# Optimization experiments

Hardware: AMD Instinct MI355X
Metric: run time of the kernel (lower is better)

Reference implementation:

```python
import jax, jax.numpy as jnp
import numpy as np
jax.config.update("jax_enable_x64", True)

B, S, E, H, L, FF = 2, 1024, 768, 12, 4, 2048
MAX_THOUGHT_LEN = 3
LN_EPS = 1e-5

def _sinusoidal_pe(max_len, d):
    pos = np.arange(max_len)[:, None]
    div = np.exp(np.arange(0, d, 2) * (-np.log(10000.0) / d))
    pe = np.zeros((max_len, d), np.float32)
    pe[:, 0::2] = np.sin(pos * div)
    pe[:, 1::2] = np.cos(pos * div)
    return jnp.asarray(pe)

def _build_mask(Smax, thoughts_taken, n_tokens):
    # Vectorized equivalent of the torch loop building the block-causal mask.
    bs = thoughts_taken + 1
    i = np.arange(Smax)[:, None]
    j = np.arange(Smax)[None, :]
    same_block = (i // bs == j // bs) & (i // bs < n_tokens) & ((i % bs) >= (j % bs))
    start_vis = ((j % bs) == 0) & (j // bs < n_tokens) & (i > j) & (i < n_tokens * bs)
    allowed = same_block | start_vis
    # TransformerEncoder canonicalizes the bool mask: True (disallowed) -> -inf additive
    return jnp.asarray(np.where(allowed, 0.0, -np.inf).astype(np.float64))

def _layernorm(x, w, b):
    mu = jnp.mean(x, -1, keepdims=True)
    var = jnp.mean((x - mu) ** 2, -1, keepdims=True)
    return (x - mu) / jnp.sqrt(var + LN_EPS) * w + b

def setup_inputs() -> dict:
    key = jax.random.key(0)
    ks = jax.random.split(key, 8)
    f32 = jnp.float32
    return {
        "x": jax.random.normal(ks[0], (B, S, E), f32),
        "padding_mask": jnp.zeros((B, S), bool),
        "thought_pe": jax.random.normal(ks[1], (MAX_THOUGHT_LEN + 1, E), f32),
        "Wqkv": jax.random.normal(ks[2], (L, 3 * E, E), f32) * (E ** -0.5),
        "bqkv": jnp.zeros((L, 3 * E), f32),
        "W1": jax.random.normal(ks[3], (L, FF, E), f32) * (E ** -0.5),
        "b1": jnp.zeros((L, FF), f32),
        "W2": jax.random.normal(ks[4], (L, E, FF), f32) * (FF ** -0.5),
        "b2": jnp.zeros((L, E), f32),
        "ln1_w": jnp.ones((L, E), f32), "ln1_b": jnp.zeros((L, E), f32),
        "ln2_w": jnp.ones((L, E), f32), "ln2_b": jnp.zeros((L, E), f32),
        "lnf_w": jnp.ones((E,), f32), "lnf_b": jnp.zeros((E,), f32),
        "thoughts_taken": 1,
        "real_token_count": 512,
    }

def reference(x, padding_mask, thought_pe, Wqkv, bqkv, W1, b1, W2, b2,
              ln1_w, ln1_b, ln2_w, ln2_b, lnf_w, lnf_b,
              thoughts_taken, real_token_count):
    # NOTE: padding_mask is accepted but unused, matching the custom layer.
    nt = thoughts_taken + 1
    pe = _sinusoidal_pe(S, E)
    # DualPositionalEncoding (eval mode -> dropout is identity)
    h = x[:, : real_token_count * nt].reshape(B, real_token_count, nt, E)
    h = h + pe[:real_token_count][None, :, None, :] + thought_pe[:nt][None, None, :, :]
    h = h.reshape(B, real_token_count * nt, E)
    pad = S - real_token_count * nt
    if pad > 0:
        h = jnp.pad(h, ((0, 0), (0, pad), (0, 0)))
    mask = _build_mask(S, thoughts_taken, real_token_count)
    scale = 1.0 / jnp.sqrt(jnp.float64(E // H))
    for l in range(L):
        # manual fp64 attention, exactly as the torch layer
        s64 = h.astype(jnp.float64)
        qkv = s64 @ Wqkv[l].astype(jnp.float64).T + bqkv[l].astype(jnp.float64)
        q, k, v = jnp.split(qkv, 3, axis=-1)
        rh = lambda t: t.reshape(B, S, H, E // H).transpose(0, 2, 1, 3)
        q, k, v = rh(q), rh(k), rh(v)
        scores = jnp.einsum("bhqd,bhkd->bhqk", q, k) * scale + mask
        attn = jax.nn.softmax(scores, axis=-1)
        ao = jnp.einsum("bhqk,bhkd->bhqd", attn, v).transpose(0, 2, 1, 3).reshape(B, S, E)
        # NOTE: no out_proj -- the custom forward skips self_attn.out_proj
        h = _layernorm(h + ao.astype(h.dtype), ln1_w[l], ln1_b[l])
        ff = jax.nn.gelu(h @ W1[l].T + b1[l], approximate=False) @ W2[l].T + b2[l]
        h = _layernorm(h + ff, ln2_w[l], ln2_b[l])
        h = jnp.nan_to_num(h)
    return _layernorm(h, lnf_w, lnf_b)
```

## Files before the change

### kernel.cpp

```cpp
#include <hip/hip_runtime.h>
#include <math.h>

#define SEQ 1024
#define EMB 768
#define NHEAD 12
#define HDIM 64
#define NLAYER 4
#define FFDIM 2048
#define BATCH 2
#define ROWS (BATCH * SEQ)
#define BH (BATCH * NHEAD)
#define NCHUNK 4

using f16 = _Float16;
using f16x4 = __attribute__((ext_vector_type(4))) _Float16;
using f16x8 = __attribute__((ext_vector_type(8))) _Float16;
using f32x4 = __attribute__((ext_vector_type(4))) float;
using f32x16 = __attribute__((ext_vector_type(16))) float;
typedef unsigned long long u64;

__device__ inline void gload16(const void* g, void* l) {
    __builtin_amdgcn_global_load_lds((const __attribute__((address_space(1))) unsigned*)g,
                                     (__attribute__((address_space(3))) unsigned*)l, 16, 0, 0);
}

__global__ void embed_kernel(const float* __restrict__ x,
                             const float* __restrict__ tpe,
                             float* __restrict__ h32,
                             f16* __restrict__ h16,
                             const int* __restrict__ tt_p,
                             const int* __restrict__ rtc_p) {
    int idx = blockIdx.x * blockDim.x + threadIdx.x;
    if (idx >= BATCH * SEQ * EMB) return;
    int e = idx % EMB;
    int s = (idx / EMB) % SEQ;
    int nt = *tt_p + 1;
    int rtc = *rtc_p;
    float val;
    if (s < rtc * nt) {
        int p = s / nt;
        int t = s % nt;
        int i2 = e & ~1;
        float div = __expf((float)i2 * -0.0119926314f);
        float ang = (float)p * div;
        float pe = (e & 1) ? __cosf(ang) : __sinf(ang);
        val = x[idx] + pe + tpe[t * EMB + e];
    } else {
        val = 0.0f;
    }
    h32[idx] = val;
    h16[idx] = (f16)val;
}

__global__ void build_mask(u64* __restrict__ mtab,
                           const int* __restrict__ tt_p,
                           const int* __restrict__ rtc_p) {
    int idx = blockIdx.x * blockDim.x + threadIdx.x;
    if (idx >= SEQ * 16) return;
    int i = idx >> 4, jt = idx & 15;
    int nt = *tt_p + 1, rtc = *rtc_p;
    int id = i / nt, im = i % nt;
    int iok = (i < rtc * nt);
    u64 m = 0;
    for (int k = 0; k < 64; k++) {
        int j = jt * 64 + k;
        int jd = j / nt, jm = j % nt;
        bool same = (id == jd) && (id < rtc) && (im >= jm);
        bool sv   = (jm == 0) && (jd < rtc) && (i > j) && iok;
        if (same || sv) m |= (1ull << k);
    }
    mtab[idx] = m;
}

__global__ void cast3(const float* __restrict__ a, int na,
                      const float* __restrict__ b, int nb,
                      const float* __restrict__ c, int nc,
                      f16* __restrict__ oa, f16* __restrict__ ob, f16* __restrict__ oc) {
    int total = na + nb + nc;
    for (int i = blockIdx.x * blockDim.x + threadIdx.x; i < total;
         i += gridDim.x * blockDim.x) {
        const float* src;
        f16* dst;
        int off;
        if (i < na)            { src = a; dst = oa; off = i; }
        else if (i < na + nb)  { src = b; dst = ob; off = i - na; }
        else                   { src = c; dst = oc; off = i - na - nb; }
        float4 v = ((const float4*)src)[off];
        f16x4 o;
        o[0] = (f16)v.x; o[1] = (f16)v.y; o[2] = (f16)v.z; o[3] = (f16)v.w;
        ((f16x4*)dst)[off] = o;
    }
}

template<int ACT, int OUT>
__global__ __launch_bounds__(256) void gemm_f16(const f16* __restrict__ A,
                                                const f16* __restrict__ W,
                                                const float* __restrict__ bias,
                                                f16* __restrict__ Ch,
                                                f16* __restrict__ vtg,
                                                int M, int N, int K) {
    __shared__ f16 As[2][128 * 64];
    __shared__ f16 Ws[2][128 * 64];
    const int tid = threadIdx.x, lane = tid & 63, wave = tid >> 6;
    const int gx = gridDim.x;
    const int nwg = gx * gridDim.y;
    int orig = blockIdx.y * gx + blockIdx.x;
    int nid = (nwg & 7) ? orig : ((orig & 7) * (nwg >> 3) + (orig >> 3));
    const int bm = (nid / gx) * 128, bn = (nid % gx) * 128;
    const int l31 = lane & 31, l32 = lane >> 5;
    const int wm = (wave >> 1) * 64, wn = (wave & 1) * 64;
    const int srow = lane >> 3, sslot = lane & 7;
    const int klen = K / gridDim.z;
    const int kbeg = blockIdx.z * klen;
    const int nsteps = klen >> 6;

    f32x16 acc[2][2];
#pragma unroll
    for (int mi = 0; mi < 2; mi++)
#pragma unroll
        for (int ni = 0; ni < 2; ni++)
#pragma unroll
            for (int e = 0; e < 16; e++) acc[mi][ni][e] = 0.f;

#pragma unroll
    for (int i = 0; i < 4; i++) {
        int R0 = wave * 32 + i * 8;
        int row = R0 + srow;
        int gs = (sslot ^ (row & 7)) << 3;
        gload16(A + (size_t)(bm + row) * K + kbeg + gs, As[0] + R0 * 64);
        gload16(W + (size_t)(bn + row) * K + kbeg + gs, Ws[0] + R0 * 64);
    }
    __syncthreads();

    int cur = 0;
    for (int t = 0; t < nsteps; t++) {
        if (t + 1 < nsteps) {
            int k1 = kbeg + (t + 1) * 64;
            int nxt = cur ^ 1;
#pragma unroll
            for (int i = 0; i < 4; i++) {
                int R0 = wave * 32 + i * 8;
                int row = R0 + srow;
                int gs = (sslot ^ (row & 7)) << 3;
                gload16(A + (size_t)(bm + row) * K + k1 + gs, As[nxt] + R0 * 64);
                gload16(W + (size_t)(bn + row) * K + k1 + gs, Ws[nxt] + R0 * 64);
            }
        }
#pragma unroll
        for (int ks = 0; ks < 4; ks++) {
            int kslot = ks * 2 + l32;
            f16x8 a[2], b[2];
#pragma unroll
            for (int mi = 0; mi < 2; mi++) {
                int row = wm + mi * 32 + l31;
                a[mi] = *(const f16x8*)(As[cur] + row * 64 + ((kslot ^ (row & 7)) << 3));
            }
#pragma unroll
            for (int ni = 0; ni < 2; ni++) {
                int row = wn + ni * 32 + l31;
                b[ni] = *(const f16x8*)(Ws[cur] + row * 64 + ((kslot ^ (row & 7)) << 3));
            }
#pragma unroll
            for (int mi = 0; mi < 2; mi++)
#pragma unroll
                for (int ni = 0; ni < 2; ni++)
                    acc[mi][ni] = __builtin_amdgcn_mfma_f32_32x32x16_f16(a[mi], b[ni], acc[mi][ni], 0, 0, 0);
        }
        __syncthreads();
        cur ^= 1;
    }

#pragma unroll
    for (int ni = 0; ni < 2; ni++) {
        int nbase = bn + wn + ni * 32;
        int n = nbase + l31;
        if (OUT == 3) {
            f16* dst = Ch + (size_t)blockIdx.z * ROWS * N;
#pragma unroll
            for (int mi = 0; mi < 2; mi++)
#pragma unroll
                for (int reg = 0; reg < 16; reg++) {
                    int m = bm + wm + mi * 32 + (reg & 3) + 8 * (reg >> 2) + 4 * l32;
                    dst[(size_t)m * N + n] = (f16)acc[mi][ni][reg];
                }
        } else {
            float bv = bias[n];
            if (OUT != 2 || nbase < 2 * EMB) {
                int cstride = (OUT == 2) ? 2 * EMB : N;
#pragma unroll
                for (int mi = 0; mi < 2; mi++) {
#pragma unroll
                    for (int reg = 0; reg < 16; reg++) {
                        int m = bm + wm + mi * 32 + (reg & 3) + 8 * (reg >> 2) + 4 * l32;
                        float v = acc[mi][ni][reg] + bv;
                        if (ACT) v = 0.5f * v * (1.0f + erff(v * 0.70710678118654752f));
                        Ch[(size_t)m * cstride + n] = (f16)v;
                    }
                }
            } else {
                int d = n - 2 * EMB;
                int hh = d >> 6, dd = d & 63;
#pragma unroll
                for (int mi = 0; mi < 2; mi++) {
#pragma unroll
                    for (int q = 0; q < 4; q++) {
                        int m0 = bm + wm + mi * 32 + 8 * q + 4 * l32;
                        int bb = m0 >> 10, s0 = m0 & (SEQ - 1);
                        f16x4 pack;
#pragma unroll
                        for (int r = 0; r < 4; r++) pack[r] = (f16)(acc[mi][ni][4 * q + r] + bv);
                        *(f16x4*)(vtg + ((size_t)((bb * NHEAD + hh) * HDIM + dd)) * SEQ + s0) = pack;
                    }
                }
            }
        }
    }
}

__global__ __launch_bounds__(256) void attn_part(const f16* __restrict__ qk,
                                                 const f16* __restrict__ vtg,
                                                 const u64* __restrict__ mtab,
                                                 f16* __restrict__ po,
                                                 float* __restrict__ pm,
                                                 float* __restrict__ pl) {
    const int c = blockIdx.x;
    const int qt = blockIdx.y;
    if (c * 4 > qt) return;
    const int bh = blockIdx.z;
    const int b = bh / NHEAD, hh = bh % NHEAD;
    const int q0 = qt * 64;
    const int jt_beg = c * 4, jt_end = min(qt, c * 4 + 3);

    __shared__ f16 Qs[64 * 64];
    __shared__ f16 Ks[2][64 * 64];
    __shared__ f16 VT[2][64 * 64];
    __shared__ f16 Ps[4 * 16 * 64];

    const int tid = threadIdx.x, lane = tid & 63, wave = tid >> 6;
    const int l15 = lane & 15, l16 = lane >> 4;
    const int RS = 2 * EMB;
    const f16* vth = vtg + (size_t)(b * NHEAD + hh) * HDIM * SEQ;
    const float SCALE2 = 0.125f * 1.44269504088896f;

#pragma unroll
    for (int it = 0; it < 2; it++) {
        int R0 = wave * 16 + it * 8;
        int row = R0 + (lane >> 3), slot = lane & 7;
        int gs = (slot ^ (row & 7)) << 3;
        gload16(qk + (size_t)(b * SEQ + q0 + row) * RS + hh * HDIM + gs, Qs + R0 * 64);
        gload16(qk + (size_t)(b * SEQ + jt_beg * 64 + row) * RS + EMB + hh * HDIM + gs,
                Ks[0] + R0 * 64);
        gload16(vth + (size_t)row * SEQ + jt_beg * 64 + gs, VT[0] + R0 * 64);
    }
    __syncthreads();

    f16x8 qa[2];
#pragma unroll
    for (int ks = 0; ks < 2; ks++) {
        int row = wave * 16 + l15;
        int kslot = l16 + ks * 4;
        qa[ks] = *(const f16x8*)(Qs + row * 64 + ((kslot ^ (row & 7)) << 3));
    }

    float mrow[4], lsum[4];
    f32x4 o[4];
    int iglob[4];
#pragma unroll
    for (int r = 0; r < 4; r++) {
        mrow[r] = -1e30f; lsum[r] = 0.f;
        iglob[r] = q0 + wave * 16 + l16 * 4 + r;
    }
#pragma unroll
    for (int nf = 0; nf < 4; nf++) o[nf] = (f32x4){0.f, 0.f, 0.f, 0.f};

    for (int jt = jt_beg; jt <= jt_end; jt++) {
        const int cur = (jt - jt_beg) & 1;
        if (jt < jt_end) {
            const int nxt = cur ^ 1;
            const int jn0 = (jt + 1) * 64;
#pragma unroll
            for (int it = 0; it < 2; it++) {
                int R0 = wave * 16 + it * 8;
                int row = R0 + (lane >> 3), slot = lane & 7;
                int gs = (slot ^ (row & 7)) << 3;
                gload16(qk + (size_t)(b * SEQ + jn0 + row) * RS + EMB + hh * HDIM + gs,
                        Ks[nxt] + R0 * 64);
                gload16(vth + (size_t)row * SEQ + jn0 + gs, VT[nxt] + R0 * 64);
            }
        }

        unsigned mlo[4], mhi[4];
#pragma unroll
        for (int r = 0; r < 4; r++) {
            u64 mk = mtab[iglob[r] * 16 + jt];
            mlo[r] = (unsigned)mk;
            mhi[r] = (unsigned)(mk >> 32);
        }

        f32x4 s[4];
        __builtin_amdgcn_s_setprio(1);
#pragma unroll
        for (int nf = 0; nf < 4; nf++) {
            s[nf] = (f32x4){0.f, 0.f, 0.f, 0.f};
#pragma unroll
            for (int ks = 0; ks < 2; ks++) {
                int row = nf * 16 + l15;
                int kslot = l16 + ks * 4;
                f16x8 kb = *(const f16x8*)(Ks[cur] + row * 64 + ((kslot ^ (row & 7)) << 3));
                s[nf] = __builtin_amdgcn_mfma_f32_16x16x32_f16(qa[ks], kb, s[nf], 0, 0, 0);
            }
        }
        __builtin_amdgcn_s_setprio(0);

        float p[4][4];
        float tmax[4] = {-1e30f, -1e30f, -1e30f, -1e30f};
#pragma unroll
        for (int nf = 0; nf < 4; nf++) {
            int sh = (nf & 1) * 16 + l15;
#pragma unroll
            for (int r = 0; r < 4; r++) {
                unsigned w = (nf & 2) ? mhi[r] : mlo[r];
                bool allowed = (w >> sh) & 1;
                float val = allowed ? s[nf][r] * SCALE2 : -1e30f;
                p[nf][r] = val;
                tmax[r] = fmaxf(tmax[r], val);
            }
        }
#pragma unroll
        for (int r = 0; r < 4; r++) {
            tmax[r] = fmaxf(tmax[r], __shfl_xor(tmax[r], 1));
            tmax[r] = fmaxf(tmax[r], __shfl_xor(tmax[r], 2));
            tmax[r] = fmaxf(tmax[r], __shfl_xor(tmax[r], 4));
            tmax[r] = fmaxf(tmax[r], __shfl_xor(tmax[r], 8));
        }
        float alpha[4], rsum[4], meff[4];
#pragma unroll
        for (int r = 0; r < 4; r++) {
            float mn = fmaxf(mrow[r], tmax[r]);
            alpha[r] = exp2f(mrow[r] - mn);
            mrow[r] = mn;
            meff[r] = (mn <= -1e29f) ? 0.f : mn;
            rsum[r] = 0.f;
        }
#pragma unroll
        for (int nf = 0; nf < 4; nf++)
#pragma unroll
            for (int r = 0; r < 4; r++) {
                float e = exp2f(p[nf][r] - meff[r]);
                p[nf][r] = e;
                rsum[r] += e;
            }
#pragma unroll
        for (int r = 0; r < 4; r++) {
            rsum[r] += __shfl_xor(rsum[r], 1);
            rsum[r] += __shfl_xor(rsum[r], 2);
            rsum[r] += __shfl_xor(rsum[r], 4);
            rsum[r] += __shfl_xor(rsum[r], 8);
            lsum[r] = lsum[r] * alpha[r] + rsum[r];
        }
#pragma unroll
        for (int nf = 0; nf < 4; nf++)
#pragma unroll
            for (int r = 0; r < 4; r++) o[nf][r] *= alpha[r];

        f16* P = Ps + wave * 16 * 64;
#pragma unroll
        for (int nf = 0; nf < 4; nf++)
#pragma unroll
            for (int r = 0; r < 4; r++) {
                int prow = l16 * 4 + r;
                int pcol = nf * 16 + l15;
                P[prow * 64 + (((pcol >> 3) ^ (prow & 7)) << 3) + (pcol & 7)] = (f16)p[nf][r];
            }

        __builtin_amdgcn_s_setprio(1);
#pragma unroll
        for (int ks = 0; ks < 2; ks++) {
            int kslot = l16 + ks * 4;
            int prow = l15;
            f16x8 pa = *(const f16x8*)(P + prow * 64 + ((kslot ^ (prow & 7)) << 3));
#pragma unroll
            for (int nf = 0; nf < 4; nf++) {
                int vrow = nf * 16 + l15;
                f16x8 vb = *(const f16x8*)(VT[cur] + vrow * 64 + ((kslot ^ (vrow & 7)) << 3));
                o[nf] = __builtin_amdgcn_mfma_f32_16x16x32_f16(pa, vb, o[nf], 0, 0, 0);
            }
        }
        __builtin_amdgcn_s_setprio(0);
        __syncthreads();
    }

    const size_t base = (size_t)(c * BH + bh) * SEQ;
#pragma unroll
    for (int r = 0; r < 4; r++) {
        int i = q0 + wave * 16 + l16 * 4 + r;
#pragma unroll
        for (int nf = 0; nf < 4; nf++)
            po[(base + i) * 64 + nf * 16 + l15] = (f16)o[nf][r];
        if (l15 == 0) {
            pm[base + i] = mrow[r];
            pl[base + i] = lsum[r];
        }
    }
}

__global__ __launch_bounds__(256) void add_ln_attn(const float* __restrict__ X,
                                                   const f16* __restrict__ po,
                                                   const float* __restrict__ pm,
                                                   const float* __restrict__ pl,
                                                   const float* __restrict__ w,
                                                   const float* __restrict__ bsh,
                                                   float* __restrict__ out32,
                                                   f16* __restrict__ out16) {
    const int row = blockIdx.x * 4 + (threadIdx.x >> 6);
    const int lane = threadIdx.x & 63;
    const int b = row >> 10, i = row & (SEQ - 1);
    const int nch = (i >> 6) / 4 + 1;
    const float* xr = X + (size_t)row * EMB;
    float4 v[3];
    float s = 0.f;
#pragma unroll
    for (int t = 0; t < 3; t++) {
        int e = t * 256 + lane * 4;
        int hh = e >> 6, d = e & 63;
        size_t hbase = (size_t)(b * NHEAD + hh) * SEQ + i;
        float m = -1e30f;
        for (int c = 0; c < nch; c++) m = fmaxf(m, pm[hbase + (size_t)c * BH * SEQ]);
        float meff = (m <= -1e29f) ? 0.f : m;
        float lt = 0.f;
        float4 ov = {0.f, 0.f, 0.f, 0.f};
        for (int c = 0; c < nch; c++) {
            size_t idx = hbase + (size_t)c * BH * SEQ;
            float wgt = exp2f(pm[idx] - meff);
            lt += pl[idx] * wgt;
            f16x4 pv = *(const f16x4*)(po + idx * 64 + d);
            ov.x += (float)pv[0] * wgt; ov.y += (float)pv[1] * wgt;
            ov.z += (float)pv[2] * wgt; ov.w += (float)pv[3] * wgt;
        }
        float inv = (lt > 0.f) ? 1.0f / lt : 0.0f;
        float4 a = *(const float4*)(xr + e);
        a.x += ov.x * inv; a.y += ov.y * inv; a.z += ov.z * inv; a.w += ov.w * inv;
        v[t] = a;
        s += a.x + a.y + a.z + a.w;
    }
#pragma unroll
    for (int k = 1; k < 64; k <<= 1) s += __shfl_xor(s, k);
    float mu = s * (1.0f / EMB);
    float s2 = 0.f;
#pragma unroll
    for (int t = 0; t < 3; t++) {
        float dx = v[t].x - mu, dy = v[t].y - mu, dz = v[t].z - mu, dw = v[t].w - mu;
        s2 += dx * dx + dy * dy + dz * dz + dw * dw;
    }
#pragma unroll
    for (int k = 1; k < 64; k <<= 1) s2 += __shfl_xor(s2, k);
    float inv = rsqrtf(s2 * (1.0f / EMB) + 1e-5f);
#pragma unroll
    for (int t = 0; t < 3; t++) {
        int e = t * 256 + lane * 4;
        float4 wv = *(const float4*)(w + e);
        float4 bv = *(const float4*)(bsh + e);
        float4 o;
        o.x = (v[t].x - mu) * inv * wv.x + bv.x;
        o.y = (v[t].y - mu) * inv * wv.y + bv.y;
        o.z = (v[t].z - mu) * inv * wv.z + bv.z;
        o.w = (v[t].w - mu) * inv * wv.w + bv.w;
        *(float4*)(out32 + (size_t)row * EMB + e) = o;
        f16x4 hh;
        hh[0] = (f16)o.x; hh[1] = (f16)o.y; hh[2] = (f16)o.z; hh[3] = (f16)o.w;
        *(f16x4*)(out16 + (size_t)row * EMB + e) = hh;
    }
}

__global__ __launch_bounds__(256) void add_ln_split4(const float* __restrict__ X,
                                                     const f16* __restrict__ part,
                                                     const float* __restrict__ bias,
                                                     const float* __restrict__ w,
                                                     const float* __restrict__ bsh,
                                                     float* __restrict__ out32,
                                                     f16* __restrict__ out16) {
    const int row = blockIdx.x * 4 + (threadIdx.x >> 6);
    const int lane = threadIdx.x & 63;
    const float* xr = X + (size_t)row * EMB;
    float4 v[3];
    float s = 0.f;
#pragma unroll
    for (int t = 0; t < 3; t++) {
        int e = t * 256 + lane * 4;
        float4 a = *(const float4*)(xr + e);
        float4 bb = *(const float4*)(bias + e);
        a.x += bb.x; a.y += bb.y; a.z += bb.z; a.w += bb.w;
#pragma unroll
        for (int z = 0; z < 4; z++) {
            f16x4 pz = *(const f16x4*)(part + (size_t)z * ROWS * EMB + (size_t)row * EMB + e);
            a.x += (float)pz[0]; a.y += (float)pz[1];
            a.z += (float)pz[2]; a.w += (float)pz[3];
        }
        v[t] = a;
        s += a.x + a.y + a.z + a.w;
    }
#pragma unroll
    for (int k = 1; k < 64; k <<= 1) s += __shfl_xor(s, k);
    float mu = s * (1.0f / EMB);
    float s2 = 0.f;
#pragma unroll
    for (int t = 0; t < 3; t++) {
        float dx = v[t].x - mu, dy = v[t].y - mu, dz = v[t].z - mu, dw = v[t].w - mu;
        s2 += dx * dx + dy * dy + dz * dz + dw * dw;
    }
#pragma unroll
    for (int k = 1; k < 64; k <<= 1) s2 += __shfl_xor(s2, k);
    float inv = rsqrtf(s2 * (1.0f / EMB) + 1e-5f);
#pragma unroll
    for (int t = 0; t < 3; t++) {
        int e = t * 256 + lane * 4;
        float4 wv = *(const float4*)(w + e);
        float4 bv = *(const float4*)(bsh + e);
        float4 o;
        o.x = (v[t].x - mu) * inv * wv.x + bv.x;
        o.y = (v[t].y - mu) * inv * wv.y + bv.y;
        o.z = (v[t].z - mu) * inv * wv.z + bv.z;
        o.w = (v[t].w - mu) * inv * wv.w + bv.w;
        *(float4*)(out32 + (size_t)row * EMB + e) = o;
        f16x4 hh;
        hh[0] = (f16)o.x; hh[1] = (f16)o.y; hh[2] = (f16)o.z; hh[3] = (f16)o.w;
        *(f16x4*)(out16 + (size_t)row * EMB + e) = hh;
    }
}

__global__ __launch_bounds__(256) void ln_final(const float* __restrict__ X,
                                                const float* __restrict__ w,
                                                const float* __restrict__ bsh,
                                                float* __restrict__ out32) {
    const int row = blockIdx.x * 4 + (threadIdx.x >> 6);
    const int lane = threadIdx.x & 63;
    const float* xr = X + (size_t)row * EMB;
    float4 v[3];
    float s = 0.f;
#pragma unroll
    for (int t = 0; t < 3; t++) {
        int e = t * 256 + lane * 4;
        v[t] = *(const float4*)(xr + e);
        s += v[t].x + v[t].y + v[t].z + v[t].w;
    }
#pragma unroll
    for (int k = 1; k < 64; k <<= 1) s += __shfl_xor(s, k);
    float mu = s * (1.0f / EMB);
    float s2 = 0.f;
#pragma unroll
    for (int t = 0; t < 3; t++) {
        float dx = v[t].x - mu, dy = v[t].y - mu, dz = v[t].z - mu, dw = v[t].w - mu;
        s2 += dx * dx + dy * dy + dz * dz + dw * dw;
    }
#pragma unroll
    for (int k = 1; k < 64; k <<= 1) s2 += __shfl_xor(s2, k);
    float inv = rsqrtf(s2 * (1.0f / EMB) + 1e-5f);
#pragma unroll
    for (int t = 0; t < 3; t++) {
        int e = t * 256 + lane * 4;
        float4 wv = *(const float4*)(w + e);
        float4 bv = *(const float4*)(bsh + e);
        float4 o;
        o.x = (v[t].x - mu) * inv * wv.x + bv.x;
        o.y = (v[t].y - mu) * inv * wv.y + bv.y;
        o.z = (v[t].z - mu) * inv * wv.z + bv.z;
        o.w = (v[t].w - mu) * inv * wv.w + bv.w;
        *(float4*)(out32 + (size_t)row * EMB + e) = o;
    }
}

extern "C" void kernel_launch(void* const* d_in, const int* in_sizes, int n_in,
                              void* d_out, int out_size, void* d_ws, size_t ws_size,
                              hipStream_t stream) {
    const float* x      = (const float*)d_in[0];
    const float* tpe    = (const float*)d_in[2];
    const float* Wqkv   = (const float*)d_in[3];
    const float* bqkv   = (const float*)d_in[4];
    const float* W1     = (const float*)d_in[5];
    const float* b1     = (const float*)d_in[6];
    const float* W2     = (const float*)d_in[7];
    const float* b2     = (const float*)d_in[8];
    const float* ln1_w  = (const float*)d_in[9];
    const float* ln1_b  = (const float*)d_in[10];
    const float* ln2_w  = (const float*)d_in[11];
    const float* ln2_b  = (const float*)d_in[12];
    const float* lnf_w  = (const float*)d_in[13];
    const float* lnf_b  = (const float*)d_in[14];
    const int*   tt     = (const int*)d_in[15];
    const int*   rtc    = (const int*)d_in[16];
    float* out = (float*)d_out;

    char* wsp = (char*)d_ws;
    float* h32  = (float*)wsp;
    f16*   h16  = (f16*)(wsp + 6291456);
    f16*   act  = (f16*)(wsp + 9437184);
    f16*   vtg  = (f16*)(wsp + 17825792);
    f16*   part = (f16*)(wsp + 20971520);
    f16*   wbuf = (f16*)(wsp + 33554432);
    f16*   po   = (f16*)(wsp + 72876032);
    float* pm   = (float*)(wsp + 85458944);
    float* pl   = (float*)(wsp + 85852160);
    u64*   mtab = (u64*)(wsp + 86245376);

    const int EQ = 3 * EMB * EMB;
    const int E1 = FFDIM * EMB;
    const int E2 = EMB * FFDIM;
    f16* wqAll = wbuf;
    f16* w1All = wbuf + (size_t)NLAYER * EQ;
    f16* w2All = w1All + (size_t)NLAYER * E1;

    cast3<<<4096, 256, 0, stream>>>(Wqkv, NLAYER * EQ / 4, W1, NLAYER * E1 / 4,
                                    W2, NLAYER * E2 / 4, wqAll, w1All, w2All);
    embed_kernel<<<(BATCH * SEQ * EMB + 255) / 256, 256, 0, stream>>>(x, tpe, h32, h16, tt, rtc);
    build_mask<<<SEQ * 16 / 256, 256, 0, stream>>>(mtab, tt, rtc);

    for (int l = 0; l < NLAYER; l++) {
        const f16* wq16 = wqAll + (size_t)l * EQ;
        const f16* w116 = w1All + (size_t)l * E1;
        const f16* w216 = w2All + (size_t)l * E2;
        const float* bq  = bqkv + (size_t)l * 3 * EMB;
        const float* bb1 = b1 + (size_t)l * FFDIM;
        const float* bb2 = b2 + (size_t)l * EMB;

        gemm_f16<0, 2><<<dim3(3 * EMB / 128, ROWS / 128), 256, 0, stream>>>(
            h16, wq16, bq, act, vtg, ROWS, 3 * EMB, EMB);

        attn_part<<<dim3(NCHUNK, SEQ / 64, BH), 256, 0, stream>>>(act, vtg, mtab, po, pm, pl);

        add_ln_attn<<<ROWS / 4, 256, 0, stream>>>(h32, po, pm, pl,
                                                  ln1_w + l * EMB, ln1_b + l * EMB, h32, h16);

        gemm_f16<1, 1><<<dim3(FFDIM / 128, ROWS / 128), 256, 0, stream>>>(
            h16, w116, bb1, act, nullptr, ROWS, FFDIM, EMB);

        gemm_f16<0, 3><<<dim3(EMB / 128, ROWS / 128, 4), 256, 0, stream>>>(
            act, w216, nullptr, part, nullptr, ROWS, EMB, FFDIM);

        add_ln_split4<<<ROWS / 4, 256, 0, stream>>>(h32, part, bb2,
                                                    ln2_w + l * EMB, ln2_b + l * EMB, h32, h16);
    }

    ln_final<<<ROWS / 4, 256, 0, stream>>>(h32, lnf_w, lnf_b, out);
}
```

Baseline: 450.2 us.

## Fuse prep kernels, fold final LayerNorm, and halve attention key-chunk count

Merges weight casting, embedding and mask building into one prep launch, and folds the final LayerNorm into the last layer's add+LN kernel. This removes three launches and one full pass over the hidden state. It also changes attention split-K from 4 chunks of 4 key tiles to 2 chunks of 8 tiles. That means fewer partials to merge in add_ln_attn, but less parallelism for long query rows.

```diff
diff --git a/kernel.cpp b/kernel.cpp
--- a/kernel.cpp
+++ b/kernel.cpp
@@ -10,7 +10,8 @@
 #define BATCH 2
 #define ROWS (BATCH * SEQ)
 #define BH (BATCH * NHEAD)
-#define NCHUNK 4
+#define NCHUNK 2
+#define CTILES 8
 
 using f16 = _Float16;
 using f16x4 = __attribute__((ext_vector_type(4))) _Float16;
@@ -24,71 +25,69 @@
                                      (__attribute__((address_space(3))) unsigned*)l, 16, 0, 0);
 }
 
-__global__ void embed_kernel(const float* __restrict__ x,
-                             const float* __restrict__ tpe,
-                             float* __restrict__ h32,
-                             f16* __restrict__ h16,
-                             const int* __restrict__ tt_p,
-                             const int* __restrict__ rtc_p) {
-    int idx = blockIdx.x * blockDim.x + threadIdx.x;
-    if (idx >= BATCH * SEQ * EMB) return;
-    int e = idx % EMB;
-    int s = (idx / EMB) % SEQ;
-    int nt = *tt_p + 1;
-    int rtc = *rtc_p;
-    float val;
-    if (s < rtc * nt) {
-        int p = s / nt;
-        int t = s % nt;
-        int i2 = e & ~1;
-        float div = __expf((float)i2 * -0.0119926314f);
-        float ang = (float)p * div;
-        float pe = (e & 1) ? __cosf(ang) : __sinf(ang);
-        val = x[idx] + pe + tpe[t * EMB + e];
-    } else {
-        val = 0.0f;
-    }
-    h32[idx] = val;
-    h16[idx] = (f16)val;
-}
-
-__global__ void build_mask(u64* __restrict__ mtab,
-                           const int* __restrict__ tt_p,
-                           const int* __restrict__ rtc_p) {
-    int idx = blockIdx.x * blockDim.x + threadIdx.x;
-    if (idx >= SEQ * 16) return;
-    int i = idx >> 4, jt = idx & 15;
-    int nt = *tt_p + 1, rtc = *rtc_p;
-    int id = i / nt, im = i % nt;
-    int iok = (i < rtc * nt);
-    u64 m = 0;
-    for (int k = 0; k < 64; k++) {
-        int j = jt * 64 + k;
-        int jd = j / nt, jm = j % nt;
-        bool same = (id == jd) && (id < rtc) && (im >= jm);
-        bool sv   = (jm == 0) && (jd < rtc) && (i > j) && iok;
-        if (same || sv) m |= (1ull << k);
-    }
-    mtab[idx] = m;
-}
-
-__global__ void cast3(const float* __restrict__ a, int na,
-                      const float* __restrict__ b, int nb,
-                      const float* __restrict__ c, int nc,
-                      f16* __restrict__ oa, f16* __restrict__ ob, f16* __restrict__ oc) {
-    int total = na + nb + nc;
+__global__ void prep_kernel(const float* __restrict__ Wq, int na,
+                            const float* __restrict__ W1, int nb,
+                            const float* __restrict__ W2, int nc,
+                            f16* __restrict__ oq, f16* __restrict__ o1, f16* __restrict__ o2,
+                            const float* __restrict__ x,
+                            const float* __restrict__ tpe,
+                            float* __restrict__ h32,
+                            f16* __restrict__ h16,
+                            u64* __restrict__ mtab,
+                            const int* __restrict__ tt_p,
+                            const int* __restrict__ rtc_p) {
+    const int ncast = na + nb + nc;
+    const int nembed = BATCH * SEQ * EMB;
+    const int nmask = SEQ * 16;
+    const int total = ncast + nembed + nmask;
+    const int nt = *tt_p + 1;
+    const int rtc = *rtc_p;
     for (int i = blockIdx.x * blockDim.x + threadIdx.x; i < total;
          i += gridDim.x * blockDim.x) {
-        const float* src;
-        f16* dst;
-        int off;
-        if (i < na)            { src = a; dst = oa; off = i; }
-        else if (i < na + nb)  { src = b; dst = ob; off = i - na; }
-        else                   { src = c; dst = oc; off = i - na - nb; }
-        float4 v = ((const float4*)src)[off];
-        f16x4 o;
-        o[0] = (f16)v.x; o[1] = (f16)v.y; o[2] = (f16)v.z; o[3] = (f16)v.w;
-        ((f16x4*)dst)[off] = o;
+        if (i < ncast) {
+            const float* src;
+            f16* dst;
+            int off;
+            if (i < na)            { src = Wq; dst = oq; off = i; }
+            else if (i < na + nb)  { src = W1; dst = o1; off = i - na; }
+            else                   { src = W2; dst = o2; off = i - na - nb; }
+            float4 v = ((const float4*)src)[off];
+            f16x4 o;
+            o[0] = (f16)v.x; o[1] = (f16)v.y; o[2] = (f16)v.z; o[3] = (f16)v.w;
+            ((f16x4*)dst)[off] = o;
+        } else if (i < ncast + nembed) {
+            int idx = i - ncast;
+            int e = idx % EMB;
+            int s = (idx / EMB) % SEQ;
+            float val;
+            if (s < rtc * nt) {
+                int p = s / nt;
+                int t = s % nt;
+                int i2 = e & ~1;
+                float div = __expf((float)i2 * -0.0119926314f);
+                float ang = (float)p * div;
+                float pe = (e & 1) ? __cosf(ang) : __sinf(ang);
+                val = x[idx] + pe + tpe[t * EMB + e];
+            } else {
+                val = 0.0f;
+            }
+            h32[idx] = val;
+            h16[idx] = (f16)val;
+        } else {
+            int idx = i - ncast - nembed;
+            int ii = idx >> 4, jt = idx & 15;
+            int id = ii / nt, im = ii % nt;
+            int iok = (ii < rtc * nt);
+            u64 m = 0;
+            for (int k = 0; k < 64; k++) {
+                int j = jt * 64 + k;
+                int jd = j / nt, jm = j % nt;
+                bool same = (id == jd) && (id < rtc) && (im >= jm);
+                bool sv   = (jm == 0) && (jd < rtc) && (ii > j) && iok;
+                if (same || sv) m |= (1ull << k);
+            }
+            mtab[idx] = m;
+        }
     }
 }
 
@@ -225,11 +224,11 @@
                                                  float* __restrict__ pl) {
     const int c = blockIdx.x;
     const int qt = blockIdx.y;
-    if (c * 4 > qt) return;
+    if (c * CTILES > qt) return;
     const int bh = blockIdx.z;
     const int b = bh / NHEAD, hh = bh % NHEAD;
     const int q0 = qt * 64;
-    const int jt_beg = c * 4, jt_end = min(qt, c * 4 + 3);
+    const int jt_beg = c * CTILES, jt_end = min(qt, c * CTILES + CTILES - 1);
 
     __shared__ f16 Qs[64 * 64];
     __shared__ f16 Ks[2][64 * 64];
@@ -415,7 +414,7 @@
     const int row = blockIdx.x * 4 + (threadIdx.x >> 6);
     const int lane = threadIdx.x & 63;
     const int b = row >> 10, i = row & (SEQ - 1);
-    const int nch = (i >> 6) / 4 + 1;
+    const int nch = (i >> 6) / CTILES + 1;
     const float* xr = X + (size_t)row * EMB;
     float4 v[3];
     float s = 0.f;
@@ -472,11 +471,14 @@
     }
 }
 
+template<int FINAL>
 __global__ __launch_bounds__(256) void add_ln_split4(const float* __restrict__ X,
                                                      const f16* __restrict__ part,
                                                      const float* __restrict__ bias,
                                                      const float* __restrict__ w,
                                                      const float* __restrict__ bsh,
+                                                     const float* __restrict__ wf,
+                                                     const float* __restrict__ bf,
                                                      float* __restrict__ out32,
                                                      f16* __restrict__ out16) {
     const int row = blockIdx.x * 4 + (threadIdx.x >> 6);
@@ -511,6 +513,8 @@
 #pragma unroll
     for (int k = 1; k < 64; k <<= 1) s2 += __shfl_xor(s2, k);
     float inv = rsqrtf(s2 * (1.0f / EMB) + 1e-5f);
+    float4 o2[3];
+    float sF = 0.f;
 #pragma unroll
     for (int t = 0; t < 3; t++) {
         int e = t * 256 + lane * 4;
@@ -521,51 +525,40 @@
         o.y = (v[t].y - mu) * inv * wv.y + bv.y;
         o.z = (v[t].z - mu) * inv * wv.z + bv.z;
         o.w = (v[t].w - mu) * inv * wv.w + bv.w;
-        *(float4*)(out32 + (size_t)row * EMB + e) = o;
-        f16x4 hh;
-        hh[0] = (f16)o.x; hh[1] = (f16)o.y; hh[2] = (f16)o.z; hh[3] = (f16)o.w;
-        *(f16x4*)(out16 + (size_t)row * EMB + e) = hh;
-    }
-}
-
-__global__ __launch_bounds__(256) void ln_final(const float* __restrict__ X,
-                                                const float* __restrict__ w,
-                                                const float* __restrict__ bsh,
-                                                float* __restrict__ out32) {
-    const int row = blockIdx.x * 4 + (threadIdx.x >> 6);
-    const int lane = threadIdx.x & 63;
-    const float* xr = X + (size_t)row * EMB;
-    float4 v[3];
-    float s = 0.f;
-#pragma unroll
-    for (int t = 0; t < 3; t++) {
-        int e = t * 256 + lane * 4;
-        v[t] = *(const float4*)(xr + e);
-        s += v[t].x + v[t].y + v[t].z + v[t].w;
-    }
-#pragma unroll
-    for (int k = 1; k < 64; k <<= 1) s += __shfl_xor(s, k);
-    float mu = s * (1.0f / EMB);
-    float s2 = 0.f;
-#pragma unroll
-    for (int t = 0; t < 3; t++) {
-        float dx = v[t].x - mu, dy = v[t].y - mu, dz = v[t].z - mu, dw = v[t].w - mu;
-        s2 += dx * dx + dy * dy + dz * dz + dw * dw;
-    }
-#pragma unroll
-    for (int k = 1; k < 64; k <<= 1) s2 += __shfl_xor(s2, k);
-    float inv = rsqrtf(s2 * (1.0f / EMB) + 1e-5f);
-#pragma unroll
-    for (int t = 0; t < 3; t++) {
-        int e = t * 256 + lane * 4;
-        float4 wv = *(const float4*)(w + e);
-        float4 bv = *(const float4*)(bsh + e);
-        float4 o;
-        o.x = (v[t].x - mu) * inv * wv.x + bv.x;
-        o.y = (v[t].y - mu) * inv * wv.y + bv.y;
-        o.z = (v[t].z - mu) * inv * wv.z + bv.z;
-        o.w = (v[t].w - mu) * inv * wv.w + bv.w;
-        *(float4*)(out32 + (size_t)row * EMB + e) = o;
+        o2[t] = o;
+        if (FINAL) sF += o.x + o.y + o.z + o.w;
+        else {
+            *(float4*)(out32 + (size_t)row * EMB + e) = o;
+            f16x4 hh;
+            hh[0] = (f16)o.x; hh[1] = (f16)o.y; hh[2] = (f16)o.z; hh[3] = (f16)o.w;
+            *(f16x4*)(out16 + (size_t)row * EMB + e) = hh;
+        }
+    }
+    if (FINAL) {
+#pragma unroll
+        for (int k = 1; k < 64; k <<= 1) sF += __shfl_xor(sF, k);
+        float muF = sF * (1.0f / EMB);
+        float s2F = 0.f;
+#pragma unroll
+        for (int t = 0; t < 3; t++) {
+            float dx = o2[t].x - muF, dy = o2[t].y - muF, dz = o2[t].z - muF, dw = o2[t].w - muF;
+            s2F += dx * dx + dy * dy + dz * dz + dw * dw;
+        }
+#pragma unroll
+        for (int k = 1; k < 64; k <<= 1) s2F += __shfl_xor(s2F, k);
+        float invF = rsqrtf(s2F * (1.0f / EMB) + 1e-5f);
+#pragma unroll
+        for (int t = 0; t < 3; t++) {
+            int e = t * 256 + lane * 4;
+            float4 wv = *(const float4*)(wf + e);
+            float4 bv = *(const float4*)(bf + e);
+            float4 o;
+            o.x = (o2[t].x - muF) * invF * wv.x + bv.x;
+            o.y = (o2[t].y - muF) * invF * wv.y + bv.y;
+            o.z = (o2[t].z - muF) * invF * wv.z + bv.z;
+            o.w = (o2[t].w - muF) * invF * wv.w + bv.w;
+            *(float4*)(out32 + (size_t)row * EMB + e) = o;
+        }
     }
 }
 
@@ -598,9 +591,9 @@
     f16*   part = (f16*)(wsp + 20971520);
     f16*   wbuf = (f16*)(wsp + 33554432);
     f16*   po   = (f16*)(wsp + 72876032);
-    float* pm   = (float*)(wsp + 85458944);
-    float* pl   = (float*)(wsp + 85852160);
-    u64*   mtab = (u64*)(wsp + 86245376);
+    float* pm   = (float*)(wsp + 79167488);
+    float* pl   = (float*)(wsp + 79364096);
+    u64*   mtab = (u64*)(wsp + 79560704);
 
     const int EQ = 3 * EMB * EMB;
     const int E1 = FFDIM * EMB;
@@ -609,10 +602,9 @@
     f16* w1All = wbuf + (size_t)NLAYER * EQ;
     f16* w2All = w1All + (size_t)NLAYER * E1;
 
-    cast3<<<4096, 256, 0, stream>>>(Wqkv, NLAYER * EQ / 4, W1, NLAYER * E1 / 4,
-                                    W2, NLAYER * E2 / 4, wqAll, w1All, w2All);
-    embed_kernel<<<(BATCH * SEQ * EMB + 255) / 256, 256, 0, stream>>>(x, tpe, h32, h16, tt, rtc);
-    build_mask<<<SEQ * 16 / 256, 256, 0, stream>>>(mtab, tt, rtc);
+    prep_kernel<<<4096, 256, 0, stream>>>(Wqkv, NLAYER * EQ / 4, W1, NLAYER * E1 / 4,
+                                          W2, NLAYER * E2 / 4, wqAll, w1All, w2All,
+                                          x, tpe, h32, h16, mtab, tt, rtc);
 
     for (int l = 0; l < NLAYER; l++) {
         const f16* wq16 = wqAll + (size_t)l * EQ;
@@ -636,9 +628,11 @@
         gemm_f16<0, 3><<<dim3(EMB / 128, ROWS / 128, 4), 256, 0, stream>>>(
             act, w216, nullptr, part, nullptr, ROWS, EMB, FFDIM);
 
-        add_ln_split4<<<ROWS / 4, 256, 0, stream>>>(h32, part, bb2,
-                                                    ln2_w + l * EMB, ln2_b + l * EMB, h32, h16);
-    }
-
-    ln_final<<<ROWS / 4, 256, 0, stream>>>(h32, lnf_w, lnf_b, out);
+        if (l < NLAYER - 1)
+            add_ln_split4<0><<<ROWS / 4, 256, 0, stream>>>(h32, part, bb2,
+                ln2_w + l * EMB, ln2_b + l * EMB, nullptr, nullptr, h32, h16);
+        else
+            add_ln_split4<1><<<ROWS / 4, 256, 0, stream>>>(h32, part, bb2,
+                ln2_w + l * EMB, ln2_b + l * EMB, lnf_w, lnf_b, out, nullptr);
+    }
 }
```

After: 421.8 us. 1.07x faster.
